# Performance work log

Measured on AMD Instinct MI355X. Metric: run time of the kernel, lower is better.

Reference implementation:

```python
import jax, jax.numpy as jnp
import numpy as np
from jax import lax

H = 64            # GRU hidden size
NUM_LAYERS = 4
EPS = 1e-5        # BatchNorm eps
NEG_SLOPE = 0.1   # LeakyReLU slope


def setup_inputs() -> dict:
    key = jax.random.key(0)
    ks = jax.random.split(key, 24)
    B, T, D = 4096, 34, 180

    def u(k, shape, fan):
        s = 1.0 / np.sqrt(fan)
        return jax.random.uniform(k, shape, jnp.float32, -s, s)

    inp = {
        "poses": jax.random.normal(ks[0], (B, T, D), jnp.float32),
        # pre_conv: Conv1d(180,16,3) -> BN(16) -> Conv1d(16,8,3) -> BN(8) -> Conv1d(8,8,3)
        "conv1_w": u(ks[1], (16, D, 3), D * 3),
        "conv1_b": u(ks[2], (16,), D * 3),
        "bn1_g": jnp.ones((16,), jnp.float32),
        "bn1_b": jnp.zeros((16,), jnp.float32),
        "conv2_w": u(ks[3], (8, 16, 3), 16 * 3),
        "conv2_b": u(ks[4], (8,), 16 * 3),
        "bn2_g": jnp.ones((8,), jnp.float32),
        "bn2_b": jnp.zeros((8,), jnp.float32),
        "conv3_w": u(ks[5], (8, 8, 3), 8 * 3),
        "conv3_b": u(ks[6], (8,), 8 * 3),
        # GRU layer 0: input 8 -> hidden 64
        "gru0_w_ih": u(ks[7], (3 * H, 8), H),
        # GRU layers 1..3: input 64 -> hidden 64 (stacked)
        "gru_w_ih": u(ks[8], (NUM_LAYERS - 1, 3 * H, H), H),
        "gru_w_hh": u(ks[9], (NUM_LAYERS, 3 * H, H), H),
        "gru_b_ih": u(ks[10], (NUM_LAYERS, 3 * H), H),
        "gru_b_hh": u(ks[11], (NUM_LAYERS, 3 * H), H),
        "out_w": u(ks[12], (1, H), H),
        "out_b": u(ks[13], (1,), H),
        "out2_w": u(ks[14], (1, T - 6), T - 6),
        "out2_b": u(ks[15], (1,), T - 6),
    }
    return inp


def _conv1d(x, w, b):
    # x: [B, C_in, L], w: [C_out, C_in, K] -> [B, C_out, L-K+1]
    y = lax.conv_general_dilated(x, w, (1,), 'VALID',
                                 dimension_numbers=('NCH', 'OIH', 'NCH'))
    return y + b[None, :, None]


def _bn_train(x, g, b):
    # training-mode BatchNorm1d over (batch, length) per channel; x: [B, C, L]
    m = jnp.mean(x, axis=(0, 2), keepdims=True)
    v = jnp.mean(jnp.square(x - m), axis=(0, 2), keepdims=True)  # biased var
    return (x - m) * jax.lax.rsqrt(v + EPS) * g[None, :, None] + b[None, :, None]


def _leaky(x):
    return jnp.where(x >= 0, x, NEG_SLOPE * x)


def _gru_layer(x_tbh, w_ih, w_hh, b_ih, b_hh):
    # x_tbh: [T, B, D_in]; returns outputs [T, B, H]
    xg = jnp.einsum('tbi,gi->tbg', x_tbh, w_ih) + b_ih  # [T, B, 3H]

    def step(h, xg_t):
        hg = h @ w_hh.T + b_hh
        i_r, i_z, i_n = jnp.split(xg_t, 3, axis=-1)
        h_r, h_z, h_n = jnp.split(hg, 3, axis=-1)
        r = jax.nn.sigmoid(i_r + h_r)
        z = jax.nn.sigmoid(i_z + h_z)
        n = jnp.tanh(i_n + r * h_n)
        h_new = n - n * z + z * h  # == (1-z)*n + z*h
        return h_new, h_new

    B = x_tbh.shape[1]
    h0 = jnp.zeros((B, H), x_tbh.dtype)
    _, ys = lax.scan(step, h0, xg)
    return ys


def reference(poses, conv1_w, conv1_b, bn1_g, bn1_b, conv2_w, conv2_b,
              bn2_g, bn2_b, conv3_w, conv3_b, gru0_w_ih, gru_w_ih,
              gru_w_hh, gru_b_ih, gru_b_hh, out_w, out_b, out2_w, out2_b):
    x = jnp.transpose(poses, (0, 2, 1))          # [B, D, T]
    x = _leaky(_bn_train(_conv1d(x, conv1_w, conv1_b), bn1_g, bn1_b))
    x = _leaky(_bn_train(_conv1d(x, conv2_w, conv2_b), bn2_g, bn2_b))
    x = _conv1d(x, conv3_w, conv3_b)             # [B, 8, T-6]
    feat = jnp.transpose(x, (2, 0, 1))           # [T', B, 8] time-major

    out = _gru_layer(feat, gru0_w_ih, gru_w_hh[0], gru_b_ih[0], gru_b_hh[0])
    for i in range(1, NUM_LAYERS):
        out = _gru_layer(out, gru_w_ih[i - 1], gru_w_hh[i], gru_b_ih[i], gru_b_hh[i])

    out = jnp.transpose(out, (1, 0, 2))          # [B, T', H]
    y = jnp.einsum('bth,oh->bto', out, out_w)[..., 0] + out_b[0]  # [B, T']
    y = y @ out2_w[0] + out2_b[0]                # [B]
    return jax.nn.sigmoid(y)[:, None]            # [B, 1]
```

## Files before the change

### kernel.cpp

```cpp
#include <hip/hip_runtime.h>

typedef unsigned short u16;
typedef __attribute__((ext_vector_type(8))) short bf16x8;
typedef __attribute__((ext_vector_type(4))) short bf16x4;
typedef __attribute__((ext_vector_type(4))) float f32x4;

#define TP 28
#define NB 4096

__device__ __forceinline__ u16 f2bf(float x) {
  union { float f; unsigned u; } v; v.f = x;
  unsigned u = v.u;
  return (u16)((u + 0x7fffu + ((u >> 16) & 1u)) >> 16);
}
__device__ __forceinline__ float bf2f(u16 h) {
  union { unsigned u; float f; } v; v.u = ((unsigned)h) << 16; return v.f;
}
#if __has_builtin(__builtin_amdgcn_rcpf)
__device__ __forceinline__ float rcp_(float x) { return __builtin_amdgcn_rcpf(x); }
#else
__device__ __forceinline__ float rcp_(float x) {
  float r;
  asm("v_rcp_f32 %0, %1" : "=v"(r) : "v"(x));
  return r;
}
#endif
__device__ __forceinline__ float sigm(float x) { return rcp_(1.0f + __expf(-x)); }
__device__ __forceinline__ float tanh_(float x) { return 1.0f - 2.0f * rcp_(1.0f + __expf(2.0f * x)); }
__device__ __forceinline__ float leaky(float x) { return x >= 0.0f ? x : 0.1f * x; }
__device__ __forceinline__ f32x4 mfma16(bf16x8 a, bf16x8 b, f32x4 c) {
  return __builtin_amdgcn_mfma_f32_16x16x32_bf16(a, b, c, 0, 0, 0);
}
__device__ __forceinline__ bf16x8 pack8(float4 a, float4 b) {
  bf16x8 f;
  f[0] = (short)f2bf(a.x); f[1] = (short)f2bf(a.y);
  f[2] = (short)f2bf(a.z); f[3] = (short)f2bf(a.w);
  f[4] = (short)f2bf(b.x); f[5] = (short)f2bf(b.y);
  f[6] = (short)f2bf(b.z); f[7] = (short)f2bf(b.w);
  return f;
}
__device__ __forceinline__ bf16x8 ldfrag8(const float* p) {
  float4 u0 = *(const float4*)p;
  float4 u1 = *(const float4*)(p + 4);
  return pack8(u0, u1);
}

__global__ __launch_bounds__(256, 3) void k_conv1(
    const float* __restrict__ poses, const float* __restrict__ w1,
    const float* __restrict__ b1, float* __restrict__ y1,
    float* __restrict__ p1)
{
  __shared__ __align__(16) u16 xs[2][6128];
  __shared__ __align__(16) u16 wt[16][544];
  __shared__ float sp[4][16];
  __shared__ float sq[4][16];
  const int tid = threadIdx.x;
  for (int i = tid; i < 16 * 544; i += 256) ((u16*)wt)[i] = 0;
  if (tid < 16) xs[tid >> 3][6120 + (tid & 7)] = 0;
  __syncthreads();
  for (int i = tid; i < 8640; i += 256) {
    int co = i / 540, r = i % 540, ci = r / 3, tap = r % 3;
    wt[co][tap * 180 + ci] = f2bf(w1[i]);
  }
  const int b0 = blockIdx.x * 2;
  {
    const float4* s4 = (const float4*)(poses + (size_t)b0 * 6120);
    for (int i = tid; i < 3060; i += 256) {
      float4 v = s4[i];
      int bb = i / 1530, p4 = i - bb * 1530;
      unsigned lo = (unsigned)f2bf(v.x) | ((unsigned)f2bf(v.y) << 16);
      unsigned hi = (unsigned)f2bf(v.z) | ((unsigned)f2bf(v.w) << 16);
      *(uint2*)&xs[bb][p4 * 4] = make_uint2(lo, hi);
    }
  }
  __syncthreads();

  const int lane = tid & 63;
  const int wv = tid >> 6;
  const int co = lane & 15;
  const int kgrp = lane >> 4;
  const int kg = kgrp * 8;
  const int R0 = kgrp * 4;
  const int bb = wv >> 1;
  const int b = b0 + bb;
  const int t0 = (wv & 1) * 16;
  const u16* pr = &xs[bb][(t0 + co) * 180];
  const float bias = b1[co];
  f32x4 acc = {bias, bias, bias, bias};

#pragma unroll
  for (int s = 0; s < 17; ++s) {
    bf16x4 lo = *(const bf16x4*)(pr + s * 32 + kg);
    bf16x4 hi = *(const bf16x4*)(pr + s * 32 + kg + 4);
    bf16x8 a0 = {lo[0], lo[1], lo[2], lo[3], hi[0], hi[1], hi[2], hi[3]};
    bf16x8 wf = *(const bf16x8*)&wt[co][s * 32 + kg];
    acc = mfma16(a0, wf, acc);
  }

  float s_ = 0.f, q_ = 0.f;
#pragma unroll
  for (int r = 0; r < 4; ++r) { s_ += acc[r]; q_ += acc[r] * acc[r]; }
  *(float4*)(y1 + (size_t)b * 512 + co * 32 + t0 + R0) =
      make_float4(acc[0], acc[1], acc[2], acc[3]);
  s_ += __shfl_xor(s_, 16); q_ += __shfl_xor(q_, 16);
  s_ += __shfl_xor(s_, 32); q_ += __shfl_xor(q_, 32);
  if (lane < 16) { sp[wv][co] = s_; sq[wv][co] = q_; }
  __syncthreads();
  if (tid < 32) {
    int ss = tid >> 4, c = tid & 15;
    float v = ss ? (sq[0][c] + sq[1][c] + sq[2][c] + sq[3][c])
                 : (sp[0][c] + sp[1][c] + sp[2][c] + sp[3][c]);
    p1[blockIdx.x * 32 + ss * 16 + c] = v;
  }
}

__global__ __launch_bounds__(1024) void k_stats1(
    const float* __restrict__ p1, const float* __restrict__ g,
    const float* __restrict__ bb, float* __restrict__ sc)
{
  __shared__ float red[32][32];
  __shared__ float tot[32];
  const int tid = threadIdx.x;
  const int col = tid & 31, rg = tid >> 5;
  float a = 0;
  for (int r = rg; r < 2048; r += 32) a += p1[r * 32 + col];
  red[rg][col] = a;
  __syncthreads();
  if (tid < 32) {
    float t = 0;
    for (int i = 0; i < 32; ++i) t += red[i][tid];
    tot[tid] = t;
  }
  __syncthreads();
  if (tid < 16) {
    const float inv = 1.0f / 131072.0f;
    float m = tot[tid] * inv;
    float var = tot[16 + tid] * inv - m * m;
    float s = g[tid] * rsqrtf(fmaxf(var, 0.0f) + 1e-5f);
    sc[tid] = s;
    sc[16 + tid] = bb[tid] - m * s;
  }
}

__global__ __launch_bounds__(256) void k_conv2(
    const float* __restrict__ y1, const float* __restrict__ sc,
    const float* __restrict__ w2, const float* __restrict__ b2,
    float* __restrict__ y2, float* __restrict__ p2)
{
  __shared__ float a1[8][16][33];
  __shared__ float w2s[384];
  __shared__ float sp[4][8][2];
  const int tid = threadIdx.x;
  const int b0 = blockIdx.x * 8;
  for (int i = tid; i < 384; i += 256) w2s[i] = w2[i];
  for (int i = tid; i < 4096; i += 256) {
    int bb = i >> 9, c = (i >> 5) & 15, t = i & 31;
    float v = y1[(size_t)(b0 + bb) * 512 + c * 32 + t] * sc[c] + sc[16 + c];
    a1[bb][c][t] = leaky(v);
  }
  __syncthreads();
  float acc[8];
  const int bb = tid / 30, t = tid % 30;
  const bool act = tid < 240;
#pragma unroll
  for (int co = 0; co < 8; ++co) acc[co] = act ? b2[co] : 0.0f;
  if (act) {
    for (int ci = 0; ci < 16; ++ci) {
      float x0 = a1[bb][ci][t], x1 = a1[bb][ci][t + 1], x2 = a1[bb][ci][t + 2];
#pragma unroll
      for (int co = 0; co < 8; ++co) {
        const float* wp = &w2s[co * 48 + ci * 3];
        acc[co] += x0 * wp[0] + x1 * wp[1] + x2 * wp[2];
      }
    }
    for (int co = 0; co < 8; ++co)
      y2[(size_t)(b0 + bb) * 240 + co * 30 + t] = acc[co];
  }
  const int w = tid >> 6;
#pragma unroll
  for (int co = 0; co < 8; ++co) {
    float s = act ? acc[co] : 0.0f;
    float q = s * s;
#pragma unroll
    for (int m = 1; m <= 32; m <<= 1) { s += __shfl_xor(s, m); q += __shfl_xor(q, m); }
    if ((tid & 63) == 0) { sp[w][co][0] = s; sp[w][co][1] = q; }
  }
  __syncthreads();
  if (tid < 16) {
    int s = tid >> 3, c = tid & 7;
    p2[blockIdx.x * 16 + s * 8 + c] = sp[0][c][s] + sp[1][c][s] + sp[2][c][s] + sp[3][c][s];
  }
}

__global__ __launch_bounds__(256) void k_stats2(
    const float* __restrict__ p2, const float* __restrict__ g,
    const float* __restrict__ bb, float* __restrict__ sc)
{
  __shared__ float red[16][16];
  __shared__ float tot[16];
  const int tid = threadIdx.x;
  const int col = tid & 15, r0 = tid >> 4;
  float a = 0;
  for (int r = r0; r < 512; r += 16) a += p2[r * 16 + col];
  red[r0][col] = a;
  __syncthreads();
  if (tid < 16) {
    float t = 0;
    for (int i = 0; i < 16; ++i) t += red[i][tid];
    tot[tid] = t;
  }
  __syncthreads();
  if (tid < 8) {
    const float inv = 1.0f / 122880.0f;
    float m = tot[tid] * inv;
    float var = tot[8 + tid] * inv - m * m;
    float s = g[tid] * rsqrtf(fmaxf(var, 0.0f) + 1e-5f);
    sc[32 + tid] = s;
    sc[40 + tid] = bb[tid] - m * s;
  }
}

__global__ __launch_bounds__(256) void k_conv3(
    const float* __restrict__ y2, const float* __restrict__ sc,
    const float* __restrict__ w3, const float* __restrict__ b3,
    u16* __restrict__ feat)
{
  __shared__ float a2[8][8][31];
  __shared__ float w3s[192];
  const int tid = threadIdx.x;
  const int b0 = blockIdx.x * 8;
  for (int i = tid; i < 192; i += 256) w3s[i] = w3[i];
  for (int i = tid; i < 1920; i += 256) {
    int bb = i / 240, rem = i % 240, c = rem / 30, t = rem % 30;
    float v = y2[(size_t)(b0 + bb) * 240 + c * 30 + t] * sc[32 + c] + sc[40 + c];
    a2[bb][c][t] = leaky(v);
  }
  __syncthreads();
  if (tid < 224) {
    int bb = tid / 28, t = tid % 28;
    float acc[8];
#pragma unroll
    for (int co = 0; co < 8; ++co) acc[co] = b3[co];
    for (int ci = 0; ci < 8; ++ci) {
      float x0 = a2[bb][ci][t], x1 = a2[bb][ci][t + 1], x2 = a2[bb][ci][t + 2];
#pragma unroll
      for (int co = 0; co < 8; ++co) {
        const float* wp = &w3s[co * 24 + ci * 3];
        acc[co] += x0 * wp[0] + x1 * wp[1] + x2 * wp[2];
      }
    }
    union { u16 h[8]; uint4 v; } u;
#pragma unroll
    for (int co = 0; co < 8; ++co) u.h[co] = f2bf(acc[co]);
    *(uint4*)&feat[((size_t)t * NB + b0 + bb) * 8] = u.v;
  }
}

__global__ __launch_bounds__(1024) void k_gru_pipe(
    const u16* __restrict__ feat,
    const float* __restrict__ g0wih,
    const float* __restrict__ gwih,
    const float* __restrict__ gwhh,
    const float* __restrict__ gbih,
    const float* __restrict__ gbhh,
    const float* __restrict__ ow, const float* __restrict__ ob,
    const float* __restrict__ o2w, const float* __restrict__ o2b,
    float* __restrict__ out)
{
  __shared__ __align__(16) u16 xl[2][16][40];
  __shared__ __align__(16) u16 hl[4][2][16][72];
  __shared__ float sph[4][16];
  const int tid = threadIdx.x;
  const int b0 = blockIdx.x * 16;
  const int lane = tid & 63;
  const int wv = tid >> 6;
  const int l = wv >> 2;
  const int c = wv & 3;
  const int row = lane & 15;
  const int kgrp = lane >> 4;
  const int kg = kgrp * 8;
  const int R0 = kgrp * 4;
  const int cr = c * 16 + row;

  for (int i = tid; i < 4 * 2 * 16 * 72; i += 1024) ((u16*)hl)[i] = 0;
  for (int i = tid; i < 2 * 16 * 40; i += 1024) ((u16*)xl)[i] = 0;

  bf16x8 Wx[3][2], Wh[3][2];
  if (l == 0) {
#pragma unroll
    for (int g = 0; g < 3; ++g) {
      bf16x8 z;
#pragma unroll
      for (int j = 0; j < 8; ++j) z[j] = 0;
      if (kg == 0) z = ldfrag8(g0wih + (g * 64 + cr) * 8);
      Wx[g][0] = z;
      Wx[g][1] = z;
    }
  } else {
#pragma unroll
    for (int g = 0; g < 3; ++g)
#pragma unroll
      for (int s = 0; s < 2; ++s)
        Wx[g][s] = ldfrag8(gwih + (l - 1) * 12288 + (g * 64 + cr) * 64 + s * 32 + kg);
  }
#pragma unroll
  for (int g = 0; g < 3; ++g)
#pragma unroll
    for (int s = 0; s < 2; ++s)
      Wh[g][s] = ldfrag8(gwhh + l * 12288 + (g * 64 + cr) * 64 + s * 32 + kg);

  const float br = gbih[l * 192 + cr] + gbhh[l * 192 + cr];
  const float bz = gbih[l * 192 + 64 + cr] + gbhh[l * 192 + 64 + cr];
  const float bi = gbih[l * 192 + 128 + cr];
  const float bh = gbhh[l * 192 + 128 + cr];

  float hold[4] = {0.f, 0.f, 0.f, 0.f};
  float accL[4] = {0.f, 0.f, 0.f, 0.f};
  const float owv = ow[cr];

  uint2 pf = make_uint2(0u, 0u);
  const bool xldr = (wv == 0 && lane < 32);
  if (xldr)
    pf = *(const uint2*)(feat + ((size_t)0 * NB + b0 + (lane >> 1)) * 8 + (lane & 1) * 4);
  __syncthreads();
  if (xldr)
    *(uint2*)&xl[0][lane >> 1][(lane & 1) * 4] = pf;
  __syncthreads();

  for (int tick = 0; tick < TP + 3; ++tick) {
    const int t = tick - l;
    if (t >= 0 && t < TP) {
      const int cur = t & 1, nxt = cur ^ 1;
      bf16x8 ax0, ax1, ah0, ah1;
      if (l == 0) {
        ax0 = *(const bf16x8*)&xl[cur][row][kg];
      } else {
        ax0 = *(const bf16x8*)&hl[l - 1][nxt][row][kg];
        ax1 = *(const bf16x8*)&hl[l - 1][nxt][row][32 + kg];
      }
      ah0 = *(const bf16x8*)&hl[l][cur][row][kg];
      ah1 = *(const bf16x8*)&hl[l][cur][row][32 + kg];
      if (xldr && t + 1 < TP)
        pf = *(const uint2*)(feat + ((size_t)(t + 1) * NB + b0 + (lane >> 1)) * 8 + (lane & 1) * 4);

      f32x4 ar = {br, br, br, br};
      f32x4 az = {bz, bz, bz, bz};
      f32x4 ai = {bi, bi, bi, bi};
      f32x4 an = {bh, bh, bh, bh};

      ar = mfma16(ax0, Wx[0][0], ar);
      az = mfma16(ax0, Wx[1][0], az);
      ai = mfma16(ax0, Wx[2][0], ai);
      if (l != 0) {
        ar = mfma16(ax1, Wx[0][1], ar);
        az = mfma16(ax1, Wx[1][1], az);
        ai = mfma16(ax1, Wx[2][1], ai);
      }
      ar = mfma16(ah0, Wh[0][0], ar);
      ar = mfma16(ah1, Wh[0][1], ar);
      az = mfma16(ah0, Wh[1][0], az);
      az = mfma16(ah1, Wh[1][1], az);
      an = mfma16(ah0, Wh[2][0], an);
      an = mfma16(ah1, Wh[2][1], an);

      float o2 = 0.f;
      if (l == 3) o2 = o2w[t];
      u16 hb[4];
#pragma unroll
      for (int r = 0; r < 4; ++r) {
        float rr = sigm(ar[r]);
        float zz = sigm(az[r]);
        float nn = tanh_(ai[r] + rr * an[r]);
        float hv = nn + zz * (hold[r] - nn);
        hold[r] = hv;
        hb[r] = f2bf(hv);
        if (l == 3) accL[r] += hv * owv * o2;
      }
#pragma unroll
      for (int r = 0; r < 4; ++r) hl[l][nxt][R0 + r][cr] = hb[r];
      if (xldr && t + 1 < TP)
        *(uint2*)&xl[nxt][lane >> 1][(lane & 1) * 4] = pf;
    }
    __syncthreads();
  }

  if (l == 3) {
#pragma unroll
    for (int r = 0; r < 4; ++r) {
      accL[r] += __shfl_xor(accL[r], 1);
      accL[r] += __shfl_xor(accL[r], 2);
      accL[r] += __shfl_xor(accL[r], 4);
      accL[r] += __shfl_xor(accL[r], 8);
    }
    if ((lane & 15) == 0) {
#pragma unroll
      for (int r = 0; r < 4; ++r) sph[c][R0 + r] = accL[r];
    }
  }
  __syncthreads();
  if (tid < 16) {
    float s = sph[0][tid] + sph[1][tid] + sph[2][tid] + sph[3][tid];
    float so2 = 0.f;
    for (int t = 0; t < TP; ++t) so2 += o2w[t];
    out[b0 + tid] = sigm(s + ob[0] * so2 + o2b[0]);
  }
}

extern "C" void kernel_launch(void* const* d_in, const int* in_sizes, int n_in,
                              void* d_out, int out_size, void* d_ws, size_t ws_size,
                              hipStream_t stream)
{
  const float* poses = (const float*)d_in[0];
  const float* c1w = (const float*)d_in[1];
  const float* c1b = (const float*)d_in[2];
  const float* bn1g = (const float*)d_in[3];
  const float* bn1b = (const float*)d_in[4];
  const float* c2w = (const float*)d_in[5];
  const float* c2b = (const float*)d_in[6];
  const float* bn2g = (const float*)d_in[7];
  const float* bn2b = (const float*)d_in[8];
  const float* c3w = (const float*)d_in[9];
  const float* c3b = (const float*)d_in[10];
  const float* g0wih = (const float*)d_in[11];
  const float* gwih = (const float*)d_in[12];
  const float* gwhh = (const float*)d_in[13];
  const float* gbih = (const float*)d_in[14];
  const float* gbhh = (const float*)d_in[15];
  const float* ow = (const float*)d_in[16];
  const float* ob = (const float*)d_in[17];
  const float* o2w = (const float*)d_in[18];
  const float* o2b = (const float*)d_in[19];

  float* ws = (float*)d_ws;
  float* y1 = ws;
  float* y2 = ws + 2097152;
  u16* feat = (u16*)(ws + 3080192);
  float* p1 = ws + 3538944;
  float* p2 = ws + 3604480;
  float* sc = ws + 3612672;
  float* outv = (float*)d_out;

  k_conv1<<<dim3(2048), dim3(256), 0, stream>>>(poses, c1w, c1b, y1, p1);
  k_stats1<<<dim3(1), dim3(1024), 0, stream>>>(p1, bn1g, bn1b, sc);
  k_conv2<<<dim3(512), dim3(256), 0, stream>>>(y1, sc, c2w, c2b, y2, p2);
  k_stats2<<<dim3(1), dim3(256), 0, stream>>>(p2, bn2g, bn2b, sc);
  k_conv3<<<dim3(512), dim3(256), 0, stream>>>(y2, sc, c3w, c3b, feat);
  k_gru_pipe<<<dim3(256), dim3(1024), 0, stream>>>(feat, g0wih, gwih, gwhh,
                                                   gbih, gbhh, ow, ob, o2w, o2b, outv);
}
```

Measured before the change: 130.8 us.

## Fold BN stats into conv kernels, prescale GRU weights for exp2, widen conv1

The two single-block BN statistics kernels are removed. Every conv2 and conv3 block now redundantly reduces the partial sums itself, which saves two launches at the cost of repeated global reads of the partials. GRU weights and biases are prescaled by log2(e), and by 2*log2(e) for the candidate gate, so the gates can use raw v_exp_f32. The MFMA section is wrapped with s_setprio. conv1 moves to 512 threads with the input loads issued up front, but only 4 of its 8 waves do the MFMA work.

```diff
diff --git a/kernel.cpp b/kernel.cpp
--- a/kernel.cpp
+++ b/kernel.cpp
@@ -7,6 +7,7 @@
 
 #define TP 28
 #define NB 4096
+#define L2E 1.4426950408889634f
 
 __device__ __forceinline__ u16 f2bf(float x) {
   union { float f; unsigned u; } v; v.f = x;
@@ -16,36 +17,38 @@
 __device__ __forceinline__ float bf2f(u16 h) {
   union { unsigned u; float f; } v; v.u = ((unsigned)h) << 16; return v.f;
 }
-#if __has_builtin(__builtin_amdgcn_rcpf)
-__device__ __forceinline__ float rcp_(float x) { return __builtin_amdgcn_rcpf(x); }
-#else
 __device__ __forceinline__ float rcp_(float x) {
   float r;
   asm("v_rcp_f32 %0, %1" : "=v"(r) : "v"(x));
   return r;
 }
-#endif
+__device__ __forceinline__ float exp2_(float x) {
+  float r;
+  asm("v_exp_f32 %0, %1" : "=v"(r) : "v"(x));
+  return r;
+}
+__device__ __forceinline__ float sigm2(float x) { return rcp_(1.0f + exp2_(-x)); }
+__device__ __forceinline__ float tanh2(float x) { return 1.0f - 2.0f * rcp_(1.0f + exp2_(x)); }
 __device__ __forceinline__ float sigm(float x) { return rcp_(1.0f + __expf(-x)); }
-__device__ __forceinline__ float tanh_(float x) { return 1.0f - 2.0f * rcp_(1.0f + __expf(2.0f * x)); }
 __device__ __forceinline__ float leaky(float x) { return x >= 0.0f ? x : 0.1f * x; }
 __device__ __forceinline__ f32x4 mfma16(bf16x8 a, bf16x8 b, f32x4 c) {
   return __builtin_amdgcn_mfma_f32_16x16x32_bf16(a, b, c, 0, 0, 0);
 }
-__device__ __forceinline__ bf16x8 pack8(float4 a, float4 b) {
+__device__ __forceinline__ bf16x8 pack8s(float4 a, float4 b, float s) {
   bf16x8 f;
-  f[0] = (short)f2bf(a.x); f[1] = (short)f2bf(a.y);
-  f[2] = (short)f2bf(a.z); f[3] = (short)f2bf(a.w);
-  f[4] = (short)f2bf(b.x); f[5] = (short)f2bf(b.y);
-  f[6] = (short)f2bf(b.z); f[7] = (short)f2bf(b.w);
+  f[0] = (short)f2bf(a.x * s); f[1] = (short)f2bf(a.y * s);
+  f[2] = (short)f2bf(a.z * s); f[3] = (short)f2bf(a.w * s);
+  f[4] = (short)f2bf(b.x * s); f[5] = (short)f2bf(b.y * s);
+  f[6] = (short)f2bf(b.z * s); f[7] = (short)f2bf(b.w * s);
   return f;
 }
-__device__ __forceinline__ bf16x8 ldfrag8(const float* p) {
+__device__ __forceinline__ bf16x8 ldfrag8s(const float* p, float s) {
   float4 u0 = *(const float4*)p;
   float4 u1 = *(const float4*)(p + 4);
-  return pack8(u0, u1);
-}
-
-__global__ __launch_bounds__(256, 3) void k_conv1(
+  return pack8s(u0, u1, s);
+}
+
+__global__ __launch_bounds__(512, 8) void k_conv1(
     const float* __restrict__ poses, const float* __restrict__ w1,
     const float* __restrict__ b1, float* __restrict__ y1,
     float* __restrict__ p1)
@@ -55,24 +58,31 @@
   __shared__ float sp[4][16];
   __shared__ float sq[4][16];
   const int tid = threadIdx.x;
-  for (int i = tid; i < 16 * 544; i += 256) ((u16*)wt)[i] = 0;
+  for (int i = tid; i < 16 * 544; i += 512) ((u16*)wt)[i] = 0;
   if (tid < 16) xs[tid >> 3][6120 + (tid & 7)] = 0;
   __syncthreads();
-  for (int i = tid; i < 8640; i += 256) {
+  for (int i = tid; i < 8640; i += 512) {
     int co = i / 540, r = i % 540, ci = r / 3, tap = r % 3;
     wt[co][tap * 180 + ci] = f2bf(w1[i]);
   }
+
   const int b0 = blockIdx.x * 2;
-  {
-    const float4* s4 = (const float4*)(poses + (size_t)b0 * 6120);
-    for (int i = tid; i < 3060; i += 256) {
-      float4 v = s4[i];
-      int bb = i / 1530, p4 = i - bb * 1530;
-      unsigned lo = (unsigned)f2bf(v.x) | ((unsigned)f2bf(v.y) << 16);
-      unsigned hi = (unsigned)f2bf(v.z) | ((unsigned)f2bf(v.w) << 16);
-      *(uint2*)&xs[bb][p4 * 4] = make_uint2(lo, hi);
-    }
-  }
+  const float4* s4 = (const float4*)(poses + (size_t)b0 * 6120);
+  float4 rv0, rv1, rv2, rv3, rv4, rv5;
+  rv0 = s4[tid];        rv1 = s4[512 + tid];  rv2 = s4[1024 + tid];
+  rv3 = s4[1536 + tid]; rv4 = s4[2048 + tid];
+  if (tid < 500) rv5 = s4[2560 + tid];
+#define CVW(J, RV)                                                     \
+  {                                                                    \
+    int i = (J)*512 + tid;                                             \
+    int bb_ = i / 1530, p4 = i - bb_ * 1530;                           \
+    unsigned lo = (unsigned)f2bf(RV.x) | ((unsigned)f2bf(RV.y) << 16); \
+    unsigned hi = (unsigned)f2bf(RV.z) | ((unsigned)f2bf(RV.w) << 16); \
+    *(uint2*)&xs[bb_][p4 * 4] = make_uint2(lo, hi);                    \
+  }
+  CVW(0, rv0) CVW(1, rv1) CVW(2, rv2) CVW(3, rv3) CVW(4, rv4)
+  if (tid < 500) CVW(5, rv5)
+#undef CVW
   __syncthreads();
 
   const int lane = tid & 63;
@@ -81,30 +91,31 @@
   const int kgrp = lane >> 4;
   const int kg = kgrp * 8;
   const int R0 = kgrp * 4;
-  const int bb = wv >> 1;
-  const int b = b0 + bb;
-  const int t0 = (wv & 1) * 16;
-  const u16* pr = &xs[bb][(t0 + co) * 180];
-  const float bias = b1[co];
-  f32x4 acc = {bias, bias, bias, bias};
-
-#pragma unroll
-  for (int s = 0; s < 17; ++s) {
-    bf16x4 lo = *(const bf16x4*)(pr + s * 32 + kg);
-    bf16x4 hi = *(const bf16x4*)(pr + s * 32 + kg + 4);
-    bf16x8 a0 = {lo[0], lo[1], lo[2], lo[3], hi[0], hi[1], hi[2], hi[3]};
-    bf16x8 wf = *(const bf16x8*)&wt[co][s * 32 + kg];
-    acc = mfma16(a0, wf, acc);
-  }
-
-  float s_ = 0.f, q_ = 0.f;
-#pragma unroll
-  for (int r = 0; r < 4; ++r) { s_ += acc[r]; q_ += acc[r] * acc[r]; }
-  *(float4*)(y1 + (size_t)b * 512 + co * 32 + t0 + R0) =
-      make_float4(acc[0], acc[1], acc[2], acc[3]);
-  s_ += __shfl_xor(s_, 16); q_ += __shfl_xor(q_, 16);
-  s_ += __shfl_xor(s_, 32); q_ += __shfl_xor(q_, 32);
-  if (lane < 16) { sp[wv][co] = s_; sq[wv][co] = q_; }
+
+  if (wv < 4) {
+    const int bb = wv >> 1;
+    const int b = b0 + bb;
+    const int t0 = (wv & 1) * 16;
+    const u16* pr = &xs[bb][(t0 + co) * 180];
+    const float bias = b1[co];
+    f32x4 acc = {bias, bias, bias, bias};
+#pragma unroll
+    for (int s = 0; s < 17; ++s) {
+      bf16x4 lo = *(const bf16x4*)(pr + s * 32 + kg);
+      bf16x4 hi = *(const bf16x4*)(pr + s * 32 + kg + 4);
+      bf16x8 a0 = {lo[0], lo[1], lo[2], lo[3], hi[0], hi[1], hi[2], hi[3]};
+      bf16x8 wf = *(const bf16x8*)&wt[co][s * 32 + kg];
+      acc = mfma16(a0, wf, acc);
+    }
+    float s_ = 0.f, q_ = 0.f;
+#pragma unroll
+    for (int r = 0; r < 4; ++r) { s_ += acc[r]; q_ += acc[r] * acc[r]; }
+    *(float4*)(y1 + (size_t)b * 512 + co * 32 + t0 + R0) =
+        make_float4(acc[0], acc[1], acc[2], acc[3]);
+    s_ += __shfl_xor(s_, 16); q_ += __shfl_xor(q_, 16);
+    s_ += __shfl_xor(s_, 32); q_ += __shfl_xor(q_, 32);
+    if (lane < 16) { sp[wv][co] = s_; sq[wv][co] = q_; }
+  }
   __syncthreads();
   if (tid < 32) {
     int ss = tid >> 4, c = tid & 15;
@@ -114,48 +125,47 @@
   }
 }
 
-__global__ __launch_bounds__(1024) void k_stats1(
-    const float* __restrict__ p1, const float* __restrict__ g,
-    const float* __restrict__ bb, float* __restrict__ sc)
-{
-  __shared__ float red[32][32];
-  __shared__ float tot[32];
-  const int tid = threadIdx.x;
-  const int col = tid & 31, rg = tid >> 5;
-  float a = 0;
-  for (int r = rg; r < 2048; r += 32) a += p1[r * 32 + col];
-  red[rg][col] = a;
-  __syncthreads();
-  if (tid < 32) {
-    float t = 0;
-    for (int i = 0; i < 32; ++i) t += red[i][tid];
-    tot[tid] = t;
-  }
-  __syncthreads();
-  if (tid < 16) {
-    const float inv = 1.0f / 131072.0f;
-    float m = tot[tid] * inv;
-    float var = tot[16 + tid] * inv - m * m;
-    float s = g[tid] * rsqrtf(fmaxf(var, 0.0f) + 1e-5f);
-    sc[tid] = s;
-    sc[16 + tid] = bb[tid] - m * s;
-  }
-}
-
 __global__ __launch_bounds__(256) void k_conv2(
-    const float* __restrict__ y1, const float* __restrict__ sc,
+    const float* __restrict__ y1, const float* __restrict__ p1,
+    const float* __restrict__ bn1g, const float* __restrict__ bn1b,
     const float* __restrict__ w2, const float* __restrict__ b2,
     float* __restrict__ y2, float* __restrict__ p2)
 {
+  __shared__ float red[8][32];
+  __shared__ float scs[32];
   __shared__ float a1[8][16][33];
   __shared__ float w2s[384];
   __shared__ float sp[4][8][2];
   const int tid = threadIdx.x;
+  {
+    const int col = tid & 31, rg = tid >> 5;
+    float a = 0;
+    for (int r = rg; r < 2048; r += 8) a += p1[r * 32 + col];
+    red[rg][col] = a;
+  }
+  __syncthreads();
+  if (tid < 32) {
+    float t = 0;
+#pragma unroll
+    for (int i = 0; i < 8; ++i) t += red[i][tid];
+    red[0][tid] = t;
+  }
+  __syncthreads();
+  if (tid < 16) {
+    const float inv = 1.0f / 131072.0f;
+    float m = red[0][tid] * inv;
+    float var = red[0][16 + tid] * inv - m * m;
+    float s = bn1g[tid] * rsqrtf(fmaxf(var, 0.0f) + 1e-5f);
+    scs[tid] = s;
+    scs[16 + tid] = bn1b[tid] - m * s;
+  }
+  __syncthreads();
+
   const int b0 = blockIdx.x * 8;
   for (int i = tid; i < 384; i += 256) w2s[i] = w2[i];
   for (int i = tid; i < 4096; i += 256) {
     int bb = i >> 9, c = (i >> 5) & 15, t = i & 31;
-    float v = y1[(size_t)(b0 + bb) * 512 + c * 32 + t] * sc[c] + sc[16 + c];
+    float v = y1[(size_t)(b0 + bb) * 512 + c * 32 + t] * scs[c] + scs[16 + c];
     a1[bb][c][t] = leaky(v);
   }
   __syncthreads();
@@ -192,47 +202,46 @@
   }
 }
 
-__global__ __launch_bounds__(256) void k_stats2(
-    const float* __restrict__ p2, const float* __restrict__ g,
-    const float* __restrict__ bb, float* __restrict__ sc)
-{
-  __shared__ float red[16][16];
-  __shared__ float tot[16];
-  const int tid = threadIdx.x;
-  const int col = tid & 15, r0 = tid >> 4;
-  float a = 0;
-  for (int r = r0; r < 512; r += 16) a += p2[r * 16 + col];
-  red[r0][col] = a;
-  __syncthreads();
-  if (tid < 16) {
-    float t = 0;
-    for (int i = 0; i < 16; ++i) t += red[i][tid];
-    tot[tid] = t;
-  }
-  __syncthreads();
-  if (tid < 8) {
-    const float inv = 1.0f / 122880.0f;
-    float m = tot[tid] * inv;
-    float var = tot[8 + tid] * inv - m * m;
-    float s = g[tid] * rsqrtf(fmaxf(var, 0.0f) + 1e-5f);
-    sc[32 + tid] = s;
-    sc[40 + tid] = bb[tid] - m * s;
-  }
-}
-
 __global__ __launch_bounds__(256) void k_conv3(
-    const float* __restrict__ y2, const float* __restrict__ sc,
+    const float* __restrict__ y2, const float* __restrict__ p2,
+    const float* __restrict__ bn2g, const float* __restrict__ bn2b,
     const float* __restrict__ w3, const float* __restrict__ b3,
     u16* __restrict__ feat)
 {
+  __shared__ float red[16][16];
+  __shared__ float scs[16];
   __shared__ float a2[8][8][31];
   __shared__ float w3s[192];
   const int tid = threadIdx.x;
+  {
+    const int col = tid & 15, rg = tid >> 4;
+    float a = 0;
+    for (int r = rg; r < 512; r += 16) a += p2[r * 16 + col];
+    red[rg][col] = a;
+  }
+  __syncthreads();
+  if (tid < 16) {
+    float t = 0;
+#pragma unroll
+    for (int i = 0; i < 16; ++i) t += red[i][tid];
+    red[0][tid] = t;
+  }
+  __syncthreads();
+  if (tid < 8) {
+    const float inv = 1.0f / 122880.0f;
+    float m = red[0][tid] * inv;
+    float var = red[0][8 + tid] * inv - m * m;
+    float s = bn2g[tid] * rsqrtf(fmaxf(var, 0.0f) + 1e-5f);
+    scs[tid] = s;
+    scs[8 + tid] = bn2b[tid] - m * s;
+  }
+  __syncthreads();
+
   const int b0 = blockIdx.x * 8;
   for (int i = tid; i < 192; i += 256) w3s[i] = w3[i];
   for (int i = tid; i < 1920; i += 256) {
     int bb = i / 240, rem = i % 240, c = rem / 30, t = rem % 30;
-    float v = y2[(size_t)(b0 + bb) * 240 + c * 30 + t] * sc[32 + c] + sc[40 + c];
+    float v = y2[(size_t)(b0 + bb) * 240 + c * 30 + t] * scs[c] + scs[8 + c];
     a2[bb][c][t] = leaky(v);
   }
   __syncthreads();
@@ -289,30 +298,35 @@
   if (l == 0) {
 #pragma unroll
     for (int g = 0; g < 3; ++g) {
+      const float sc_ = (g == 2) ? 2.f * L2E : L2E;
       bf16x8 z;
 #pragma unroll
       for (int j = 0; j < 8; ++j) z[j] = 0;
-      if (kg == 0) z = ldfrag8(g0wih + (g * 64 + cr) * 8);
+      if (kg == 0) z = ldfrag8s(g0wih + (g * 64 + cr) * 8, sc_);
       Wx[g][0] = z;
       Wx[g][1] = z;
     }
   } else {
 #pragma unroll
-    for (int g = 0; g < 3; ++g)
+    for (int g = 0; g < 3; ++g) {
+      const float sc_ = (g == 2) ? 2.f * L2E : L2E;
 #pragma unroll
       for (int s = 0; s < 2; ++s)
-        Wx[g][s] = ldfrag8(gwih + (l - 1) * 12288 + (g * 64 + cr) * 64 + s * 32 + kg);
-  }
-#pragma unroll
-  for (int g = 0; g < 3; ++g)
+        Wx[g][s] = ldfrag8s(gwih + (l - 1) * 12288 + (g * 64 + cr) * 64 + s * 32 + kg, sc_);
+    }
+  }
+#pragma unroll
+  for (int g = 0; g < 3; ++g) {
+    const float sc_ = (g == 2) ? 2.f * L2E : L2E;
 #pragma unroll
     for (int s = 0; s < 2; ++s)
-      Wh[g][s] = ldfrag8(gwhh + l * 12288 + (g * 64 + cr) * 64 + s * 32 + kg);
-
-  const float br = gbih[l * 192 + cr] + gbhh[l * 192 + cr];
-  const float bz = gbih[l * 192 + 64 + cr] + gbhh[l * 192 + 64 + cr];
-  const float bi = gbih[l * 192 + 128 + cr];
-  const float bh = gbhh[l * 192 + 128 + cr];
+      Wh[g][s] = ldfrag8s(gwhh + l * 12288 + (g * 64 + cr) * 64 + s * 32 + kg, sc_);
+  }
+
+  const float br = (gbih[l * 192 + cr] + gbhh[l * 192 + cr]) * L2E;
+  const float bz = (gbih[l * 192 + 64 + cr] + gbhh[l * 192 + 64 + cr]) * L2E;
+  const float bi = gbih[l * 192 + 128 + cr] * 2.f * L2E;
+  const float bh = gbhh[l * 192 + 128 + cr] * 2.f * L2E;
 
   float hold[4] = {0.f, 0.f, 0.f, 0.f};
   float accL[4] = {0.f, 0.f, 0.f, 0.f};
@@ -348,6 +362,7 @@
       f32x4 ai = {bi, bi, bi, bi};
       f32x4 an = {bh, bh, bh, bh};
 
+      __builtin_amdgcn_s_setprio(1);
       ar = mfma16(ax0, Wx[0][0], ar);
       az = mfma16(ax0, Wx[1][0], az);
       ai = mfma16(ax0, Wx[2][0], ai);
@@ -362,15 +377,16 @@
       az = mfma16(ah1, Wh[1][1], az);
       an = mfma16(ah0, Wh[2][0], an);
       an = mfma16(ah1, Wh[2][1], an);
+      __builtin_amdgcn_s_setprio(0);
 
       float o2 = 0.f;
       if (l == 3) o2 = o2w[t];
       u16 hb[4];
 #pragma unroll
       for (int r = 0; r < 4; ++r) {
-        float rr = sigm(ar[r]);
-        float zz = sigm(az[r]);
-        float nn = tanh_(ai[r] + rr * an[r]);
+        float rr = sigm2(ar[r]);
+        float zz = sigm2(az[r]);
+        float nn = tanh2(ai[r] + rr * an[r]);
         float hv = nn + zz * (hold[r] - nn);
         hold[r] = hv;
         hb[r] = f2bf(hv);
@@ -437,14 +453,11 @@
   u16* feat = (u16*)(ws + 3080192);
   float* p1 = ws + 3538944;
   float* p2 = ws + 3604480;
-  float* sc = ws + 3612672;
   float* outv = (float*)d_out;
 
-  k_conv1<<<dim3(2048), dim3(256), 0, stream>>>(poses, c1w, c1b, y1, p1);
-  k_stats1<<<dim3(1), dim3(1024), 0, stream>>>(p1, bn1g, bn1b, sc);
-  k_conv2<<<dim3(512), dim3(256), 0, stream>>>(y1, sc, c2w, c2b, y2, p2);
-  k_stats2<<<dim3(1), dim3(256), 0, stream>>>(p2, bn2g, bn2b, sc);
-  k_conv3<<<dim3(512), dim3(256), 0, stream>>>(y2, sc, c3w, c3b, feat);
+  k_conv1<<<dim3(2048), dim3(512), 0, stream>>>(poses, c1w, c1b, y1, p1);
+  k_conv2<<<dim3(512), dim3(256), 0, stream>>>(y1, p1, bn1g, bn1b, c2w, c2b, y2, p2);
+  k_conv3<<<dim3(512), dim3(256), 0, stream>>>(y2, p2, bn2g, bn2b, c3w, c3b, feat);
   k_gru_pipe<<<dim3(256), dim3(1024), 0, stream>>>(feat, g0wih, gwih, gwhh,
                                                    gbih, gbhh, ow, ob, o2w, o2b, outv);
 }
```

Measured after the change: 161.1 us. 23.2% more time.
